# Kernel tuning notes

Hardware: AMD Instinct MI355X
Metric: run time of the kernel (lower is better)

## Reference

```python
import jax, jax.numpy as jnp
import numpy as np
from jax import lax

H, V, NT, B, T = 1024, 30000, 256, 128, 50
O_ID = 1


def gru_cell(x, h, wih, whh, bih, bhh):
    # PyTorch GRU cell math
    gx = x @ wih.T + bih
    gh = h @ whh.T + bhh
    xr, xz, xn = jnp.split(gx, 3, -1)
    hr, hz, hn = jnp.split(gh, 3, -1)
    r = jax.nn.sigmoid(xr + hr)
    z = jax.nn.sigmoid(xz + hz)
    n = jnp.tanh(xn + r * hn)
    return (1.0 - z) * n + z * h


def masked_scan(xs, mask, wih, whh, bih, bhh):
    # xs [T,B,D], mask [T,B]; emulates pack_padded: padded steps keep hidden, output zeros
    Bn = xs.shape[1]
    Hn = whh.shape[1]
    h0 = jnp.zeros((Bn, Hn), xs.dtype)
    def step(h, inp):
        x, m = inp
        hn = gru_cell(x, h, wih, whh, bih, bhh)
        h_new = jnp.where(m[:, None], hn, h)
        out = jnp.where(m[:, None], hn, 0.0)
        return h_new, out
    h_fin, outs = lax.scan(step, h0, (xs, mask))
    return outs, h_fin


def reverse_padded(xs, lengths):
    # reverse each sequence within its valid length (like pack handles bidirectional)
    Tn = xs.shape[0]
    t = jnp.arange(Tn)[:, None]
    idx = jnp.clip(lengths[None, :] - 1 - t, 0, Tn - 1)  # [T,B]
    return jnp.take_along_axis(xs, idx[:, :, None], axis=0)


def bigru_layer(xs, mask, lengths, wih, whh, bih, bhh):
    out_f, h_f = masked_scan(xs, mask, wih[0], whh[0], bih[0], bhh[0])
    xs_r = reverse_padded(xs, lengths)
    out_bR, h_b = masked_scan(xs_r, mask, wih[1], whh[1], bih[1], bhh[1])
    out_b = reverse_padded(out_bR, lengths) * mask[:, :, None]
    return out_f, out_b, h_f, h_b


def reference(enc_embed, e0_wih, e0_whh, e0_bih, e0_bhh,
              e1_wih, e1_whh, e1_bih, e1_bhh,
              dec_embed, d_wih, d_whh, d_bih, d_bhh,
              concat_w, concat_b, out_w, out_b,
              input_ids, tag_ids, lengths):
    ids = input_ids.T   # [T,B]
    tags = tag_ids.T    # [T,B]
    Tn, Bn = ids.shape
    mask = jnp.arange(Tn)[:, None] < lengths[None, :]  # [T,B]

    # ---- encoder: 2-layer bi-GRU, sum fwd/bwd halves of outputs ----
    emb = enc_embed[ids]  # [T,B,H]
    of0, ob0, h0f, h0b = bigru_layer(emb, mask, lengths, e0_wih, e0_whh, e0_bih, e0_bhh)
    x1 = jnp.concatenate([of0, ob0], -1)  # [T,B,2H]
    of1, ob1, _, _ = bigru_layer(x1, mask, lengths, e1_wih, e1_whh, e1_bih, e1_bhh)
    enc_out = of1 + ob1  # [T,B,H]

    # decoder initial hidden = encoder_hidden[:2] = layer0 fwd, layer0 bwd final states
    dec_in = jnp.concatenate([jnp.full((1, Bn), O_ID, tags.dtype), tags[:-1]], 0)

    def dec_step(carry, tok):
        h0, h1 = carry
        x = dec_embed[tok]                         # [B,H]
        h0 = gru_cell(x, h0, d_wih[0], d_whh[0], d_bih[0], d_bhh[0])
        h1 = gru_cell(h0, h1, d_wih[1], d_whh[1], d_bih[1], d_bhh[1])
        rnn_out = h1
        scores = jnp.einsum('bh,tbh->bt', rnn_out, enc_out)
        attn = jax.nn.softmax(scores, -1)
        ctx = jnp.einsum('bt,tbh->bh', attn, enc_out)
        cc = jnp.tanh(jnp.concatenate([rnn_out, ctx], -1) @ concat_w.T + concat_b)
        logits = cc @ out_w.T + out_b              # [B,NT]
        return (h0, h1), logits

    _, logits = lax.scan(dec_step, (h0f, h0b), dec_in)  # [T,B,NT]

    # masked cross entropy (mean over valid tokens)
    logp = jax.nn.log_softmax(logits, -1)
    nll = -jnp.take_along_axis(logp, tags[..., None].astype(jnp.int32), -1)[..., 0]
    loss = jnp.sum(nll * mask) / jnp.sum(lengths).astype(logits.dtype)

    outputs = jnp.transpose(logits, (1, 0, 2))  # [B,T,NT]
    return outputs, loss


def setup_inputs() -> dict:
    key = jax.random.key(0)
    ks = jax.random.split(key, 24)
    s = 0.05
    inp = {
        'enc_embed': jax.random.normal(ks[0], (V, H)) * s,
        'e0_wih': jax.random.normal(ks[1], (2, 3 * H, H)) * s,
        'e0_whh': jax.random.normal(ks[2], (2, 3 * H, H)) * s,
        'e0_bih': jax.random.normal(ks[3], (2, 3 * H)) * s,
        'e0_bhh': jax.random.normal(ks[4], (2, 3 * H)) * s,
        'e1_wih': jax.random.normal(ks[5], (2, 3 * H, 2 * H)) * s,
        'e1_whh': jax.random.normal(ks[6], (2, 3 * H, H)) * s,
        'e1_bih': jax.random.normal(ks[7], (2, 3 * H)) * s,
        'e1_bhh': jax.random.normal(ks[8], (2, 3 * H)) * s,
        'dec_embed': jax.random.normal(ks[9], (NT, H)) * s,
        'd_wih': jax.random.normal(ks[10], (2, 3 * H, H)) * s,
        'd_whh': jax.random.normal(ks[11], (2, 3 * H, H)) * s,
        'd_bih': jax.random.normal(ks[12], (2, 3 * H)) * s,
        'd_bhh': jax.random.normal(ks[13], (2, 3 * H)) * s,
        'concat_w': jax.random.normal(ks[14], (H, 2 * H)) * s,
        'concat_b': jax.random.normal(ks[15], (H,)) * s,
        'out_w': jax.random.normal(ks[16], (NT, H)) * s,
        'out_b': jax.random.normal(ks[17], (NT,)) * s,
        'input_ids': jax.random.randint(ks[18], (B, T), 0, V, dtype=jnp.int32),
        'tag_ids': jax.random.randint(ks[19], (B, T), 0, NT, dtype=jnp.int32),
    }
    lengths = jax.random.randint(ks[20], (B,), 1, T + 1, dtype=jnp.int32)
    inp['lengths'] = lengths.at[0].set(T)  # max length must equal T
    return inp
```

## Files before the change

kernel.cpp:

```cpp
#include <hip/hip_runtime.h>
#include <math.h>

#define HDIM 1024
#define NTAG 256
#define BSZ 128
#define TLEN 50
#define G3 3072
#define NBLK 256
#define NGRP 8

typedef unsigned long long u64;
typedef unsigned short u16;

constexpr u64 GX_F  = (u64)TLEN*G3*BSZ;
constexpr u64 SEQ_F = (u64)TLEN*HDIM*BSZ;
constexpr u64 HST_F = (u64)HDIM*BSZ;
constexpr u64 F_GX  = 0;
constexpr u64 F_OF0 = F_GX + GX_F;
constexpr u64 F_OB0 = F_OF0 + SEQ_F;
constexpr u64 F_ENC = F_OB0 + SEQ_F;
constexpr u64 F_T0  = F_ENC + SEQ_F;
constexpr u64 F_T1  = F_T0 + HST_F;
constexpr u64 F_H0F = F_T1 + HST_F;
constexpr u64 F_H0B = F_H0F + HST_F;
constexpr u64 F_CTXF= F_H0B + HST_F;
constexpr u64 F_LG  = F_CTXF + HST_F;
constexpr u64 F_QP  = F_LG + (u64)NTAG*BSZ;
constexpr u64 F_NLL = F_QP + (u64)2*TLEN*BSZ;
constexpr u64 F_H1T = F_NLL + (u64)TLEN*BSZ;
constexpr u64 F_CWB = F_H1T + 65536;
constexpr u64 F_OWB = F_CWB + 1048576;
constexpr u64 F_ETB = F_OWB + 131072;
constexpr u64 SHU   = 65536;
constexpr u64 F_SH0A= F_ETB + 3276800;
constexpr u64 F_SH0B= F_SH0A + SHU;
constexpr u64 F_SH1A= F_SH0B + SHU;
constexpr u64 F_SH1B= F_SH1A + SHU;
constexpr u64 F_SCTX= F_SH1B + SHU;
constexpr u64 F_SCC = F_SCTX + SHU;
constexpr u64 F_SHI0= F_SCC + SHU;
constexpr u64 F_SHI1= F_SHI0 + SHU;
constexpr u64 POOL_F= F_SHI1 + SHU;

__device__ __align__(256) float g_pool[POOL_F];
__device__ unsigned g_grp[NGRP*32];
__device__ unsigned g_root;
__device__ unsigned g_gen;

__device__ __forceinline__ float sigmf(float x){ return 1.f/(1.f+__expf(-x)); }
__device__ __forceinline__ u16 f2b(float x){
  unsigned u = __float_as_uint(x);
  u += 0x7fffu + ((u>>16)&1u);
  return (u16)(u>>16);
}
__device__ __forceinline__ float b2f(u16 s){ return __uint_as_float(((unsigned)s)<<16); }
__device__ __forceinline__ float b2f_lo(unsigned p){ return __uint_as_float(p<<16); }
__device__ __forceinline__ float b2f_hi(unsigned p){ return __uint_as_float(p & 0xffff0000u); }

__device__ __forceinline__ void grid_sync(){
  __syncthreads();
  if (threadIdx.x == 0){
    const int g = blockIdx.x & (NGRP-1);
    unsigned gen = __hip_atomic_load(&g_gen, __ATOMIC_RELAXED, __HIP_MEMORY_SCOPE_AGENT);
    unsigned old = __hip_atomic_fetch_add(&g_grp[g*32], 1u, __ATOMIC_RELEASE, __HIP_MEMORY_SCOPE_AGENT);
    if (old == (NBLK/NGRP)-1){
      unsigned ro = __hip_atomic_fetch_add(&g_root, 1u, __ATOMIC_RELEASE, __HIP_MEMORY_SCOPE_AGENT);
      if (ro == NGRP-1){
        __hip_atomic_store(&g_root, 0u, __ATOMIC_RELAXED, __HIP_MEMORY_SCOPE_AGENT);
        #pragma unroll
        for (int i=0;i<NGRP;++i)
          __hip_atomic_store(&g_grp[i*32], 0u, __ATOMIC_RELAXED, __HIP_MEMORY_SCOPE_AGENT);
        __hip_atomic_fetch_add(&g_gen, 1u, __ATOMIC_RELEASE, __HIP_MEMORY_SCOPE_AGENT);
      } else {
        while (__hip_atomic_load(&g_gen, __ATOMIC_RELAXED, __HIP_MEMORY_SCOPE_AGENT) == gen)
          __builtin_amdgcn_s_sleep(4);
      }
    } else {
      while (__hip_atomic_load(&g_gen, __ATOMIC_RELAXED, __HIP_MEMORY_SCOPE_AGENT) == gen)
        __builtin_amdgcn_s_sleep(4);
    }
    (void)__hip_atomic_load(&g_gen, __ATOMIC_ACQUIRE, __HIP_MEMORY_SCOPE_AGENT);
  }
  __syncthreads();
}

__device__ __forceinline__ void ggemm12u(const u16* __restrict__ wl,
                                         const u16* __restrict__ aT,
                                         float (&acc)[12][2], int tid)
{
  const int w = tid>>6, l2 = (tid&63)*2;
  #pragma unroll
  for (int r=0;r<12;++r){ acc[r][0]=0.f; acc[r][1]=0.f; }
  const int k0 = w*128;
  const u16* ap = aT + (u64)k0*BSZ + l2;
  const u16* wp = wl + k0*12;
  for (int kb=0; kb<128; kb+=16){
    unsigned a[16];
    #pragma unroll
    for (int u=0;u<16;++u) a[u] = *(const unsigned*)(ap + (u64)(kb+u)*BSZ);
    #pragma unroll
    for (int u=0;u<16;++u){
      const u16* wr = wp + (kb+u)*12;
      const float ax = b2f_lo(a[u]), ay = b2f_hi(a[u]);
      #pragma unroll
      for (int r=0;r<12;++r){
        const float wv = b2f(wr[r]);
        acc[r][0] += wv*ax; acc[r][1] += wv*ay;
      }
    }
  }
}

__device__ __forceinline__ void reduce12(const float (&acc)[12][2], float* red, int tid){
  const int w = tid>>6, l2 = (tid&63)*2;
  __syncthreads();
  #pragma unroll
  for (int r=0;r<12;++r){
    red[(u64)(w*12+r)*128 + l2]   = acc[r][0];
    red[(u64)(w*12+r)*128 + l2+1] = acc[r][1];
  }
  __syncthreads();
}

#define AM_ENC 0
#define AM_DEC 1
#define AM_CAT 2

template<int AMODE>
__global__ __launch_bounds__(256)
void gemm_gx(const float* __restrict__ embed,
             u64 a1_f, u64 a2_f,
             const int* __restrict__ ids,
             const float* __restrict__ W,
             const float* __restrict__ bias,
             u64 c_f, int K)
{
  constexpr int TM=128, TN=64, TK=32;
  __shared__ float As[TK][TM+4];
  __shared__ float Ws[TK][TN+4];
  __shared__ int rowid[TM];
  const int t = blockIdx.x;
  const int n0 = blockIdx.y*TN;
  const int tid = threadIdx.x;

  if (AMODE != AM_CAT){
    for (int r=tid; r<TM; r+=256)
      rowid[r] = (AMODE==AM_ENC) ? ids[r*TLEN+t] : ((t==0)?1:ids[r*TLEN+t-1]);
    __syncthreads();
  }

  const int tm = tid>>4, tn = tid&15;
  float acc[8][4];
  #pragma unroll
  for (int i=0;i<8;i++){ acc[i][0]=0.f;acc[i][1]=0.f;acc[i][2]=0.f;acc[i][3]=0.f; }

  for (int k0=0;k0<K;k0+=TK){
    if (AMODE==AM_CAT){
      const int kk = tid>>3, q = tid&7;
      const int kg = k0 + kk;
      const float* src = g_pool + ((kg<HDIM)? (a1_f + ((u64)t*HDIM + kg)*BSZ)
                                            : (a2_f + ((u64)t*HDIM + (kg-HDIM))*BSZ)) + q*16;
      float* d = &As[kk][q*16];
      float4 v0=*(const float4*)(src+0), v1=*(const float4*)(src+4);
      float4 v2=*(const float4*)(src+8), v3=*(const float4*)(src+12);
      *(float4*)(d+0)=v0; *(float4*)(d+4)=v1; *(float4*)(d+8)=v2; *(float4*)(d+12)=v3;
    } else {
      #pragma unroll
      for (int l=tid; l<TM*TK; l+=256){
        int r=l>>5, k=l&31;
        As[k][r] = embed[(u64)rowid[r]*HDIM + k0 + k];
      }
    }
    #pragma unroll
    for (int l=tid; l<TN*TK; l+=256){
      int n=l>>5, k=l&31;
      Ws[k][n] = W[(u64)(n0+n)*K + k0 + k];
    }
    __syncthreads();
    #pragma unroll 8
    for (int kk=0;kk<TK;kk++){
      float4 a0 = *(const float4*)&As[kk][tm*8];
      float4 a1 = *(const float4*)&As[kk][tm*8+4];
      float4 w  = *(const float4*)&Ws[kk][tn*4];
      float av[8]={a0.x,a0.y,a0.z,a0.w,a1.x,a1.y,a1.z,a1.w};
      float wv[4]={w.x,w.y,w.z,w.w};
      #pragma unroll
      for (int i=0;i<8;i++){
        #pragma unroll
        for (int jj=0;jj<4;jj++) acc[i][jj] += av[i]*wv[jj];
      }
    }
    __syncthreads();
  }

  float bv[4];
  #pragma unroll
  for (int jj=0;jj<4;jj++) bv[jj] = bias[n0+tn*4+jj];
  float* C = g_pool + c_f;
  for (int half=0; half<2; ++half){
    if ((tn>>3)==half){
      #pragma unroll
      for (int i=0;i<8;i++)
        #pragma unroll
        for (int jj=0;jj<4;jj++)
          As[(tn&7)*4+jj][tm*8+i] = acc[i][jj]+bv[jj];
    }
    __syncthreads();
    {
      const int nn = tid>>3, q = tid&7;
      float* dst = C + ((u64)t*G3 + n0 + half*32 + nn)*BSZ + q*16;
      const float* srow = &As[nn][q*16];
      float4 v0=*(const float4*)(srow+0), v1=*(const float4*)(srow+4);
      float4 v2=*(const float4*)(srow+8), v3=*(const float4*)(srow+12);
      *(float4*)(dst+0)=v0; *(float4*)(dst+4)=v1; *(float4*)(dst+8)=v2; *(float4*)(dst+12)=v3;
    }
    __syncthreads();
  }
}

__device__ __forceinline__ void ggemm12(const u16* __restrict__ wl,
                                        const float* __restrict__ aT,
                                        float (&acc)[12][2], int tid)
{
  const int w = tid>>6, l2 = (tid&63)*2;
  #pragma unroll
  for (int r=0;r<12;++r){ acc[r][0]=0.f; acc[r][1]=0.f; }
  const int k0 = w*128;
  const float* ap = aT + (u64)k0*BSZ + l2;
  const u16* wp = wl + k0*12;
  for (int kb=0; kb<128; kb+=16){
    float2 a[16];
    #pragma unroll
    for (int u=0;u<16;++u) a[u] = *(const float2*)(ap + (u64)(kb+u)*BSZ);
    #pragma unroll
    for (int u=0;u<16;++u){
      const u16* wr = wp + (kb+u)*12;
      #pragma unroll
      for (int r=0;r<12;++r){
        const float wv = b2f(wr[r]);
        acc[r][0] += wv*a[u].x; acc[r][1] += wv*a[u].y;
      }
    }
  }
}

template<bool BWD, bool ACCUM>
__global__ __launch_bounds__(512)
void scan_kernel(u64 gx_f, u64 p0_f, u64 p1_f,
                 const float* __restrict__ whh, const float* __restrict__ bhh,
                 const int* __restrict__ lengths, u64 out_f)
{
  __shared__ u16 wl[HDIM*12];
  __shared__ float red[8*12*128];
  const int bid = blockIdx.x, tid = threadIdx.x;
  const int j0 = bid*4;
  #pragma unroll
  for (int r=0;r<12;++r){
    const int row = (r>>2)*HDIM + j0 + (r&3);
    for (int k=tid;k<HDIM;k+=512) wl[k*12+r] = f2b(whh[(u64)row*HDIM + k]);
  }
  __syncthreads();

  const int jl = tid>>7, bb = tid&127;
  const int jg = j0 + jl;
  for (int s=0; s<TLEN; ++s){
    const int t = BWD ? (TLEN-1-s) : s;
    const u64 rd = (s&1)? p0_f : p1_f;
    const u64 wr = (s&1)? p1_f : p0_f;
    if (s>0){
      float acc[12][2];
      ggemm12(wl, g_pool + rd, acc, tid);
      reduce12(acc, red, tid);
    }
    const float* gxb = g_pool + gx_f + (u64)t*G3*BSZ;
    {
      const int len = lengths[bb];
      const bool m = (t < len);
      float gh0=0.f, gh1=0.f, gh2=0.f;
      if (s>0){
        #pragma unroll
        for (int w2=0;w2<8;++w2){
          gh0 += red[(u64)(w2*12 + jl)*128 + bb];
          gh1 += red[(u64)(w2*12 + 4 + jl)*128 + bb];
          gh2 += red[(u64)(w2*12 + 8 + jl)*128 + bb];
        }
      }
      const float xr = gxb[(u64)jg*BSZ + bb];
      const float xz = gxb[(u64)(HDIM+jg)*BSZ + bb];
      const float xn = gxb[(u64)(2*HDIM+jg)*BSZ + bb];
      const float hp = (s>0)? g_pool[rd + (u64)jg*BSZ + bb] : 0.f;
      const float r = sigmf(xr + gh0 + bhh[jg]);
      const float z = sigmf(xz + gh1 + bhh[HDIM+jg]);
      const float n = tanhf(xn + r*(gh2 + bhh[2*HDIM+jg]));
      const float hv = (1.f-z)*n + z*hp;
      g_pool[wr + (u64)jg*BSZ + bb] = m ? hv : hp;
      const u64 oidx = out_f + ((u64)t*HDIM + jg)*BSZ + bb;
      if (ACCUM){ if (m) g_pool[oidx] += hv; }
      else g_pool[oidx] = m ? hv : 0.f;
    }
    grid_sync();
  }
}

__global__ __launch_bounds__(256)
void conv_w(const float* __restrict__ cw, const float* __restrict__ ow){
  u16* cwb = (u16*)(g_pool + F_CWB);
  u16* owb = (u16*)(g_pool + F_OWB);
  u16* hi0 = (u16*)(g_pool + F_SHI0);
  u16* hi1 = (u16*)(g_pool + F_SHI1);
  const u64 n1 = (u64)HDIM*2*HDIM;
  const u64 n2 = (u64)NTAG*HDIM;
  const u64 n3 = (u64)HDIM*BSZ;
  for (u64 i = (u64)blockIdx.x*256+threadIdx.x; i<n1; i += (u64)gridDim.x*256) cwb[i]=f2b(cw[i]);
  for (u64 i = (u64)blockIdx.x*256+threadIdx.x; i<n2; i += (u64)gridDim.x*256) owb[i]=f2b(ow[i]);
  for (u64 i = (u64)blockIdx.x*256+threadIdx.x; i<n3; i += (u64)gridDim.x*256){
    hi0[i]=f2b(g_pool[F_H0F + i]);
    hi1[i]=f2b(g_pool[F_H0B + i]);
  }
}
__global__ __launch_bounds__(256)
void enc_t(){
  const int t = blockIdx.x, kc = blockIdx.y;
  u16* etb = (u16*)(g_pool + F_ETB);
  for (int it=threadIdx.x; it<128*128; it+=256){
    const int kl = it>>7, b = it&127;
    const int k = kc*128 + kl;
    etb[(u64)b*(TLEN*HDIM) + (u64)t*HDIM + k] = f2b(g_pool[F_ENC + ((u64)t*HDIM+k)*BSZ + b]);
  }
}

__global__ __launch_bounds__(512)
void decoder_kernel(const float* __restrict__ whh0, const float* __restrict__ bhh0,
                    const float* __restrict__ wih1, const float* __restrict__ bih1,
                    const float* __restrict__ whh1, const float* __restrict__ bhh1,
                    const float* __restrict__ cb, const float* __restrict__ ob,
                    const int* __restrict__ tag_ids, const int* __restrict__ lengths,
                    float* __restrict__ dout)
{
  __shared__ u16 wl0[HDIM*12];
  __shared__ u16 wl1[HDIM*12];
  __shared__ u16 wl2[HDIM*12];
  __shared__ float red[8*12*128];
  __shared__ float aL[64];
  const int bid = blockIdx.x, tid = threadIdx.x;
  const int j0 = bid*4;
  const int ab = bid>>1, kh2 = bid&1;
  const int w = tid>>6, l2 = (tid&63)*2, l = tid&63;
  const int jl = tid>>7, bb = tid&127;
  const int jg = j0 + jl;

  #pragma unroll
  for (int r=0;r<12;++r){
    const int gr = (r>>2)*HDIM + j0 + (r&3);
    for (int k=tid;k<HDIM;k+=512){
      wl0[k*12+r] = f2b(whh0[(u64)gr*HDIM + k]);
      wl1[k*12+r] = f2b(wih1[(u64)gr*HDIM + k]);
      wl2[k*12+r] = f2b(whh1[(u64)gr*HDIM + k]);
    }
  }
  __syncthreads();

  u16* h1t = (u16*)(g_pool + F_H1T);
  const u16* etb = (const u16*)(g_pool + F_ETB);
  const u16* cwb = (const u16*)(g_pool + F_CWB);
  const u16* owb = (const u16*)(g_pool + F_OWB);
  u16* sctx = (u16*)(g_pool + F_SCTX);
  u16* scc  = (u16*)(g_pool + F_SCC);

  for (int t=0; t<TLEN; ++t){
    const u16* h0c = (const u16*)(g_pool + ((t==0)? F_SHI0 : ((t&1)? F_SH0A : F_SH0B)));
    u16*       h0n = (u16*)(g_pool + ((t&1)? F_SH0B : F_SH0A));
    const u16* h1c = (const u16*)(g_pool + ((t==0)? F_SHI1 : ((t&1)? F_SH1A : F_SH1B)));
    u16*       h1n = (u16*)(g_pool + ((t&1)? F_SH1B : F_SH1A));

    {
      float acc[12][2];
      ggemm12u(wl0, h0c, acc, tid);
      reduce12(acc, red, tid);
      const float* gxb = g_pool + F_GX + (u64)t*G3*BSZ;
      float gh0=0.f, gh1=0.f, gh2=0.f;
      #pragma unroll
      for (int w2=0;w2<8;++w2){
        gh0 += red[(u64)(w2*12 + jl)*128 + bb];
        gh1 += red[(u64)(w2*12 + 4 + jl)*128 + bb];
        gh2 += red[(u64)(w2*12 + 8 + jl)*128 + bb];
      }
      const float xr = gxb[(u64)jg*BSZ+bb], xz = gxb[(u64)(HDIM+jg)*BSZ+bb], xn = gxb[(u64)(2*HDIM+jg)*BSZ+bb];
      const float hp = b2f(h0c[(u64)jg*BSZ + bb]);
      const float r = sigmf(xr + gh0 + bhh0[jg]);
      const float z = sigmf(xz + gh1 + bhh0[HDIM+jg]);
      const float n = tanhf(xn + r*(gh2 + bhh0[2*HDIM+jg]));
      h0n[(u64)jg*BSZ + bb] = f2b((1.f-z)*n + z*hp);
    }
    grid_sync();

    {
      float acc[12][2];
      float aX[3], aH[3];
      ggemm12u(wl1, h0n, acc, tid);
      reduce12(acc, red, tid);
      #pragma unroll
      for (int g=0;g<3;++g){
        float s=0.f;
        #pragma unroll
        for (int w2=0;w2<8;++w2) s += red[(u64)(w2*12 + g*4 + jl)*128 + bb];
        aX[g] = s;
      }
      ggemm12u(wl2, h1c, acc, tid);
      reduce12(acc, red, tid);
      #pragma unroll
      for (int g=0;g<3;++g){
        float s=0.f;
        #pragma unroll
        for (int w2=0;w2<8;++w2) s += red[(u64)(w2*12 + g*4 + jl)*128 + bb];
        aH[g] = s;
      }
      const float hp = b2f(h1c[(u64)jg*BSZ + bb]);
      const float r = sigmf(aX[0] + bih1[jg] + aH[0] + bhh1[jg]);
      const float z = sigmf(aX[1] + bih1[HDIM+jg] + aH[1] + bhh1[HDIM+jg]);
      const float n = tanhf(aX[2] + bih1[2*HDIM+jg] + r*(aH[2] + bhh1[2*HDIM+jg]));
      const float hv = (1.f-z)*n + z*hp;
      const u16 hb = f2b(hv);
      h1n[(u64)jg*BSZ + bb] = hb;
      h1t[(u64)bb*HDIM + jg] = hb;
    }
    grid_sync();

    {
      const u16* h1r = h1t + (u64)ab*HDIM + kh2*512 + l*8;
      float hv[8];
      #pragma unroll
      for (int u=0;u<8;++u) hv[u] = b2f(h1r[u]);
      for (int tp=w; tp<TLEN; tp+=8){
        const u16* er = etb + (u64)ab*(TLEN*HDIM) + (u64)tp*HDIM + kh2*512 + l*8;
        float s=0.f;
        #pragma unroll
        for (int u=0;u<8;++u) s += hv[u]*b2f(er[u]);
        #pragma unroll
        for (int o=32;o;o>>=1) s += __shfl_xor(s, o);
        if (l==0) g_pool[F_QP + (u64)kh2*TLEN*BSZ + (u64)tp*BSZ + ab] = s;
      }
    }
    grid_sync();

    {
      if (tid < 64){
        float v = -1e30f;
        if (tid < TLEN)
          v = g_pool[F_QP + (u64)tid*BSZ + ab] + g_pool[F_QP + (u64)(TLEN+tid)*BSZ + ab];
        float mx = v;
        #pragma unroll
        for (int o=32;o;o>>=1) mx = fmaxf(mx, __shfl_xor(mx,o));
        float e = (tid<TLEN)? __expf(v-mx) : 0.f;
        float sm = e;
        #pragma unroll
        for (int o=32;o;o>>=1) sm += __shfl_xor(sm,o);
        if (tid < TLEN) aL[tid] = e/sm;
      }
      __syncthreads();
      {
        const int kk = tid;
        const u16* eb = etb + (u64)ab*(TLEN*HDIM) + kh2*512 + kk;
        float acc = 0.f;
        #pragma unroll 10
        for (int tp=0;tp<TLEN;++tp) acc += aL[tp]*b2f(eb[(u64)tp*HDIM]);
        sctx[(u64)(kh2*512+kk)*BSZ + ab] = f2b(acc);
      }
    }
    grid_sync();

    {
      const int k0 = w*256;
      const u16* asrc = (k0<1024)? ((const u16*)(g_pool + ((t&1)? F_SH1B : F_SH1A)) + (u64)k0*BSZ)
                                 : (sctx + (u64)(k0-1024)*BSZ);
      const u16* wp0 = cwb + (u64)(j0+0)*2048 + k0;
      const u16* wp1 = cwb + (u64)(j0+1)*2048 + k0;
      const u16* wp2 = cwb + (u64)(j0+2)*2048 + k0;
      const u16* wp3 = cwb + (u64)(j0+3)*2048 + k0;
      float a0[4]={0,0,0,0}, a1v[4]={0,0,0,0};
      for (int kb=0; kb<256; kb+=16){
        unsigned a[16];
        #pragma unroll
        for (int u=0;u<16;++u) a[u] = *(const unsigned*)(asrc + (u64)(kb+u)*BSZ + l2);
        #pragma unroll
        for (int u=0;u<16;++u){
          const float ax = b2f_lo(a[u]), ay = b2f_hi(a[u]);
          const float w0v=b2f(wp0[kb+u]), w1v=b2f(wp1[kb+u]), w2v=b2f(wp2[kb+u]), w3v=b2f(wp3[kb+u]);
          a0[0]+=w0v*ax; a1v[0]+=w0v*ay;
          a0[1]+=w1v*ax; a1v[1]+=w1v*ay;
          a0[2]+=w2v*ax; a1v[2]+=w2v*ay;
          a0[3]+=w3v*ax; a1v[3]+=w3v*ay;
        }
      }
      __syncthreads();
      #pragma unroll
      for (int r=0;r<4;++r){
        red[(u64)(w*4+r)*128 + l2]   = a0[r];
        red[(u64)(w*4+r)*128 + l2+1] = a1v[r];
      }
      __syncthreads();
      {
        const int n2 = j0 + jl;
        float s = cb[n2];
        #pragma unroll
        for (int w2=0;w2<8;++w2) s += red[(u64)(w2*4+jl)*128 + bb];
        scc[(u64)n2*BSZ + bb] = f2b(tanhf(s));
      }
    }
    grid_sync();

    {
      const u16* owv = owb + (u64)bid*HDIM + w*128;
      const u16* ccp = scc + (u64)w*128*BSZ;
      float a0=0.f, a1v=0.f;
      for (int kb=0; kb<128; kb+=16){
        unsigned a[16];
        #pragma unroll
        for (int u=0;u<16;++u) a[u] = *(const unsigned*)(ccp + (u64)(kb+u)*BSZ + l2);
        #pragma unroll
        for (int u=0;u<16;++u){
          const float wv = b2f(owv[kb+u]);
          a0 += wv*b2f_lo(a[u]); a1v += wv*b2f_hi(a[u]);
        }
      }
      __syncthreads();
      red[(u64)w*128 + l2]   = a0;
      red[(u64)w*128 + l2+1] = a1v;
      __syncthreads();
      if (tid < 128){
        float lg = ob[bid];
        #pragma unroll
        for (int w2=0;w2<8;++w2) lg += red[(u64)w2*128 + tid];
        g_pool[F_LG + (u64)bid*BSZ + tid] = lg;
      }
    }
    grid_sync();

    {
      float* lgs = red;
      float* rp  = red + 256;
      const bool act = (bid < BSZ) && (tid < 256);
      float lg = 0.f;
      if (act){
        lg = g_pool[F_LG + (u64)tid*BSZ + bid];
        lgs[tid] = lg; rp[tid] = lg;
      }
      __syncthreads();
      for (int o=128;o;o>>=1){ if (bid<BSZ && tid<o) rp[tid]=fmaxf(rp[tid],rp[tid+o]); __syncthreads(); }
      const float mx = (bid<BSZ)? rp[0] : 0.f;
      __syncthreads();
      if (act) rp[tid] = __expf(lg-mx);
      __syncthreads();
      for (int o=128;o;o>>=1){ if (bid<BSZ && tid<o) rp[tid]+=rp[tid+o]; __syncthreads(); }
      if (act){
        const float lse = mx + __logf(rp[0]);
        dout[((u64)bid*TLEN + t)*NTAG + tid] = lg;
        if (tid==0){
          const int tag = tag_ids[bid*TLEN + t];
          g_pool[F_NLL + (u64)t*BSZ + bid] = lse - lgs[tag];
        }
      }
    }
  }
  grid_sync();
  if (bid == 0){
    float ssum = 0.f;
    for (int i=tid; i<TLEN*BSZ; i+=512){
      const int tt = i>>7, b = i&127;
      if (tt < lengths[b]) ssum += g_pool[F_NLL + i];
    }
    red[tid] = ssum; __syncthreads();
    for (int o=256;o;o>>=1){ if (tid<o) red[tid]+=red[tid+o]; __syncthreads(); }
    if (tid==0){
      int den=0;
      for (int b=0;b<BSZ;b++) den += lengths[b];
      dout[(u64)BSZ*TLEN*NTAG] = red[0]/(float)den;
    }
  }
}

extern "C" void kernel_launch(void* const* d_in, const int* in_sizes, int n_in,
                              void* d_out, int out_size, void* d_ws, size_t ws_size,
                              hipStream_t stream)
{
  const float* enc_embed = (const float*)d_in[0];
  const float* e0_wih = (const float*)d_in[1];
  const float* e0_whh = (const float*)d_in[2];
  const float* e0_bih = (const float*)d_in[3];
  const float* e0_bhh = (const float*)d_in[4];
  const float* e1_wih = (const float*)d_in[5];
  const float* e1_whh = (const float*)d_in[6];
  const float* e1_bih = (const float*)d_in[7];
  const float* e1_bhh = (const float*)d_in[8];
  const float* dec_embed = (const float*)d_in[9];
  const float* d_wih = (const float*)d_in[10];
  const float* d_whh = (const float*)d_in[11];
  const float* d_bih = (const float*)d_in[12];
  const float* d_bhh = (const float*)d_in[13];
  const float* concat_w = (const float*)d_in[14];
  const float* concat_b = (const float*)d_in[15];
  const float* out_w = (const float*)d_in[16];
  const float* out_b = (const float*)d_in[17];
  const int* input_ids = (const int*)d_in[18];
  const int* tag_ids  = (const int*)d_in[19];
  const int* lengths  = (const int*)d_in[20];
  float* dout = (float*)d_out;

  const dim3 gxg(TLEN, G3/64);

  gemm_gx<AM_ENC><<<gxg,256,0,stream>>>(enc_embed,0,0,input_ids,e0_wih,e0_bih,F_GX,HDIM);
  scan_kernel<false,false><<<NBLK,512,0,stream>>>(F_GX, F_T0, F_H0F, e0_whh, e0_bhh, lengths, F_OF0);
  gemm_gx<AM_ENC><<<gxg,256,0,stream>>>(enc_embed,0,0,input_ids,
                                        e0_wih+(u64)G3*HDIM, e0_bih+G3, F_GX, HDIM);
  scan_kernel<true,false><<<NBLK,512,0,stream>>>(F_GX, F_T0, F_H0B,
                                        e0_whh+(u64)G3*HDIM, e0_bhh+G3, lengths, F_OB0);
  gemm_gx<AM_CAT><<<gxg,256,0,stream>>>(nullptr, F_OF0, F_OB0, nullptr,
                                        e1_wih, e1_bih, F_GX, 2*HDIM);
  scan_kernel<false,false><<<NBLK,512,0,stream>>>(F_GX, F_T0, F_T1, e1_whh, e1_bhh, lengths, F_ENC);
  gemm_gx<AM_CAT><<<gxg,256,0,stream>>>(nullptr, F_OF0, F_OB0, nullptr,
                                        e1_wih+(u64)G3*2*HDIM, e1_bih+G3, F_GX, 2*HDIM);
  scan_kernel<true,true><<<NBLK,512,0,stream>>>(F_GX, F_T0, F_T1,
                                        e1_whh+(u64)G3*HDIM, e1_bhh+G3, lengths, F_ENC);
  gemm_gx<AM_DEC><<<gxg,256,0,stream>>>(dec_embed,0,0,tag_ids, d_wih, d_bih, F_GX, HDIM);
  conv_w<<<256,256,0,stream>>>(concat_w, out_w);
  enc_t<<<dim3(TLEN,8),256,0,stream>>>();
  decoder_kernel<<<NBLK,512,0,stream>>>(d_whh, d_bhh,
                                        d_wih+(u64)G3*HDIM, d_bih+G3,
                                        d_whh+(u64)G3*HDIM, d_bhh+G3,
                                        concat_b, out_b,
                                        tag_ids, lengths, dout);
}
```

Before: 17.10 ms.

## Run forward and backward GRU scans concurrently in one paired kernel

Merges the forward and backward direction scans of each encoder layer into a single persistent launch of twice as many blocks. Each half gets its own hierarchical grid barrier, and its own gate-input and hidden-state buffers. The second layer's backward pass now writes into a separate output buffer, which the transpose kernel sums with the forward output, instead of accumulating in place. This aims to halve the number of serial latency-bound recurrence steps. The risk is that 512 blocks must all be co-resident for the spin barriers to avoid deadlock, and each CU now hosts two blocks, which adds LDS and compute pressure per step.

Result: no change. 17.09 ms (-0.1%).

```diff
diff --git a/kernel.cpp b/kernel.cpp
--- a/kernel.cpp
+++ b/kernel.cpp
@@ -16,15 +16,18 @@
 constexpr u64 SEQ_F = (u64)TLEN*HDIM*BSZ;
 constexpr u64 HST_F = (u64)HDIM*BSZ;
 constexpr u64 F_GX  = 0;
-constexpr u64 F_OF0 = F_GX + GX_F;
+constexpr u64 F_GXB = F_GX + GX_F;
+constexpr u64 F_OF0 = F_GXB + GX_F;
 constexpr u64 F_OB0 = F_OF0 + SEQ_F;
 constexpr u64 F_ENC = F_OB0 + SEQ_F;
-constexpr u64 F_T0  = F_ENC + SEQ_F;
+constexpr u64 F_ENC2= F_ENC + SEQ_F;
+constexpr u64 F_T0  = F_ENC2 + SEQ_F;
 constexpr u64 F_T1  = F_T0 + HST_F;
 constexpr u64 F_H0F = F_T1 + HST_F;
 constexpr u64 F_H0B = F_H0F + HST_F;
-constexpr u64 F_CTXF= F_H0B + HST_F;
-constexpr u64 F_LG  = F_CTXF + HST_F;
+constexpr u64 F_X0  = F_H0B + HST_F;
+constexpr u64 F_X1  = F_X0 + HST_F;
+constexpr u64 F_LG  = F_X1 + HST_F;
 constexpr u64 F_QP  = F_LG + (u64)NTAG*BSZ;
 constexpr u64 F_NLL = F_QP + (u64)2*TLEN*BSZ;
 constexpr u64 F_H1T = F_NLL + (u64)TLEN*BSZ;
@@ -46,6 +49,9 @@
 __device__ unsigned g_grp[NGRP*32];
 __device__ unsigned g_root;
 __device__ unsigned g_gen;
+__device__ unsigned g2_grp[2*NGRP*32];
+__device__ unsigned g2_root[2*32];
+__device__ unsigned g2_gen[2*32];
 
 __device__ __forceinline__ float sigmf(float x){ return 1.f/(1.f+__expf(-x)); }
 __device__ __forceinline__ u16 f2b(float x){
@@ -80,6 +86,36 @@
         __builtin_amdgcn_s_sleep(4);
     }
     (void)__hip_atomic_load(&g_gen, __ATOMIC_ACQUIRE, __HIP_MEMORY_SCOPE_AGENT);
+  }
+  __syncthreads();
+}
+
+__device__ __forceinline__ void grid_sync_h(int half){
+  __syncthreads();
+  if (threadIdx.x == 0){
+    const int g = (blockIdx.x & 255) & (NGRP-1);
+    unsigned* grp  = &g2_grp[(half*NGRP + g)*32];
+    unsigned* root = &g2_root[half*32];
+    unsigned* genp = &g2_gen[half*32];
+    unsigned gen = __hip_atomic_load(genp, __ATOMIC_RELAXED, __HIP_MEMORY_SCOPE_AGENT);
+    unsigned old = __hip_atomic_fetch_add(grp, 1u, __ATOMIC_RELEASE, __HIP_MEMORY_SCOPE_AGENT);
+    if (old == (NBLK/NGRP)-1){
+      unsigned ro = __hip_atomic_fetch_add(root, 1u, __ATOMIC_RELEASE, __HIP_MEMORY_SCOPE_AGENT);
+      if (ro == NGRP-1){
+        __hip_atomic_store(root, 0u, __ATOMIC_RELAXED, __HIP_MEMORY_SCOPE_AGENT);
+        #pragma unroll
+        for (int i=0;i<NGRP;++i)
+          __hip_atomic_store(&g2_grp[(half*NGRP + i)*32], 0u, __ATOMIC_RELAXED, __HIP_MEMORY_SCOPE_AGENT);
+        __hip_atomic_fetch_add(genp, 1u, __ATOMIC_RELEASE, __HIP_MEMORY_SCOPE_AGENT);
+      } else {
+        while (__hip_atomic_load(genp, __ATOMIC_RELAXED, __HIP_MEMORY_SCOPE_AGENT) == gen)
+          __builtin_amdgcn_s_sleep(4);
+      }
+    } else {
+      while (__hip_atomic_load(genp, __ATOMIC_RELAXED, __HIP_MEMORY_SCOPE_AGENT) == gen)
+        __builtin_amdgcn_s_sleep(4);
+    }
+    (void)__hip_atomic_load(genp, __ATOMIC_ACQUIRE, __HIP_MEMORY_SCOPE_AGENT);
   }
   __syncthreads();
 }
@@ -244,15 +280,25 @@
   }
 }
 
-template<bool BWD, bool ACCUM>
 __global__ __launch_bounds__(512)
-void scan_kernel(u64 gx_f, u64 p0_f, u64 p1_f,
-                 const float* __restrict__ whh, const float* __restrict__ bhh,
-                 const int* __restrict__ lengths, u64 out_f)
+void scan_pair(u64 gxA, u64 gxB, u64 p0A, u64 p1A, u64 p0B, u64 p1B,
+               const float* __restrict__ whhA, const float* __restrict__ whhB,
+               const float* __restrict__ bhhA, const float* __restrict__ bhhB,
+               const int* __restrict__ lengths, u64 outA, u64 outB)
 {
   __shared__ u16 wl[HDIM*12];
   __shared__ float red[8*12*128];
-  const int bid = blockIdx.x, tid = threadIdx.x;
+  const int gbid = blockIdx.x, tid = threadIdx.x;
+  const int half = gbid >> 8;
+  const int bid  = gbid & 255;
+  const u64 gx_f = half? gxB : gxA;
+  const u64 p0_f = half? p0B : p0A;
+  const u64 p1_f = half? p1B : p1A;
+  const float* whh = half? whhB : whhA;
+  const float* bhh = half? bhhB : bhhA;
+  const u64 out_f = half? outB : outA;
+  const bool bwd = (half != 0);
+
   const int j0 = bid*4;
   #pragma unroll
   for (int r=0;r<12;++r){
@@ -264,7 +310,7 @@
   const int jl = tid>>7, bb = tid&127;
   const int jg = j0 + jl;
   for (int s=0; s<TLEN; ++s){
-    const int t = BWD ? (TLEN-1-s) : s;
+    const int t = bwd ? (TLEN-1-s) : s;
     const u64 rd = (s&1)? p0_f : p1_f;
     const u64 wr = (s&1)? p1_f : p0_f;
     if (s>0){
@@ -294,11 +340,9 @@
       const float n = tanhf(xn + r*(gh2 + bhh[2*HDIM+jg]));
       const float hv = (1.f-z)*n + z*hp;
       g_pool[wr + (u64)jg*BSZ + bb] = m ? hv : hp;
-      const u64 oidx = out_f + ((u64)t*HDIM + jg)*BSZ + bb;
-      if (ACCUM){ if (m) g_pool[oidx] += hv; }
-      else g_pool[oidx] = m ? hv : 0.f;
-    }
-    grid_sync();
+      g_pool[out_f + ((u64)t*HDIM + jg)*BSZ + bb] = m ? hv : 0.f;
+    }
+    grid_sync_h(half);
   }
 }
 
@@ -325,7 +369,8 @@
   for (int it=threadIdx.x; it<128*128; it+=256){
     const int kl = it>>7, b = it&127;
     const int k = kc*128 + kl;
-    etb[(u64)b*(TLEN*HDIM) + (u64)t*HDIM + k] = f2b(g_pool[F_ENC + ((u64)t*HDIM+k)*BSZ + b]);
+    const u64 idx = ((u64)t*HDIM+k)*BSZ + b;
+    etb[(u64)b*(TLEN*HDIM) + (u64)t*HDIM + k] = f2b(g_pool[F_ENC + idx] + g_pool[F_ENC2 + idx]);
   }
 }
 
@@ -609,18 +654,18 @@
   const dim3 gxg(TLEN, G3/64);
 
   gemm_gx<AM_ENC><<<gxg,256,0,stream>>>(enc_embed,0,0,input_ids,e0_wih,e0_bih,F_GX,HDIM);
-  scan_kernel<false,false><<<NBLK,512,0,stream>>>(F_GX, F_T0, F_H0F, e0_whh, e0_bhh, lengths, F_OF0);
   gemm_gx<AM_ENC><<<gxg,256,0,stream>>>(enc_embed,0,0,input_ids,
-                                        e0_wih+(u64)G3*HDIM, e0_bih+G3, F_GX, HDIM);
-  scan_kernel<true,false><<<NBLK,512,0,stream>>>(F_GX, F_T0, F_H0B,
-                                        e0_whh+(u64)G3*HDIM, e0_bhh+G3, lengths, F_OB0);
+                                        e0_wih+(u64)G3*HDIM, e0_bih+G3, F_GXB, HDIM);
+  scan_pair<<<2*NBLK,512,0,stream>>>(F_GX, F_GXB, F_T0, F_H0F, F_T1, F_H0B,
+                                     e0_whh, e0_whh+(u64)G3*HDIM, e0_bhh, e0_bhh+G3,
+                                     lengths, F_OF0, F_OB0);
   gemm_gx<AM_CAT><<<gxg,256,0,stream>>>(nullptr, F_OF0, F_OB0, nullptr,
                                         e1_wih, e1_bih, F_GX, 2*HDIM);
-  scan_kernel<false,false><<<NBLK,512,0,stream>>>(F_GX, F_T0, F_T1, e1_whh, e1_bhh, lengths, F_ENC);
   gemm_gx<AM_CAT><<<gxg,256,0,stream>>>(nullptr, F_OF0, F_OB0, nullptr,
-                                        e1_wih+(u64)G3*2*HDIM, e1_bih+G3, F_GX, 2*HDIM);
-  scan_kernel<true,true><<<NBLK,512,0,stream>>>(F_GX, F_T0, F_T1,
-                                        e1_whh+(u64)G3*HDIM, e1_bhh+G3, lengths, F_ENC);
+                                        e1_wih+(u64)G3*2*HDIM, e1_bih+G3, F_GXB, 2*HDIM);
+  scan_pair<<<2*NBLK,512,0,stream>>>(F_GX, F_GXB, F_T0, F_X0, F_T1, F_X1,
+                                     e1_whh, e1_whh+(u64)G3*HDIM, e1_bhh, e1_bhh+G3,
+                                     lengths, F_ENC, F_ENC2);
   gemm_gx<AM_DEC><<<gxg,256,0,stream>>>(dec_embed,0,0,tag_ids, d_wih, d_bih, F_GX, HDIM);
   conv_w<<<256,256,0,stream>>>(concat_w, out_w);
   enc_t<<<dim3(TLEN,8),256,0,stream>>>();
```
